# Kernel optimization log

Measured on AMD Instinct MI355X. Metric: run time of the kernel, lower is better.

## Reference

```python
import jax, jax.numpy as jnp
import numpy as np
import math

N_EMBD = 2048
N_HEAD = 16
HEAD_DIM = N_EMBD // N_HEAD  # 128
K = 8
P = 2
B = 1
T = 2048
EPS = 1e-6


def _rms_norm(x):
    return x * jax.lax.rsqrt(jnp.mean(x * x, axis=-1, keepdims=True) + EPS)


def _rope(x, cos, sin):
    # x: [B, T, H, D]; cos/sin: [T, D//2]
    d = x.shape[-1] // 2
    x1, x2 = x[..., :d], x[..., d:]
    c = cos[None, :, None, :]
    s = sin[None, :, None, :]
    return jnp.concatenate([x1 * c + x2 * s, -x1 * s + x2 * c], axis=-1)


def setup_inputs() -> dict:
    key = jax.random.key(0)
    ks = jax.random.split(key, 8)
    x = jax.random.normal(ks[0], (B, T, N_EMBD), jnp.float32)
    half = HEAD_DIM // 2
    inv_freq = 1.0 / (10000.0 ** (np.arange(half, dtype=np.float32) / half))
    ang = np.arange(T, dtype=np.float32)[:, None] * inv_freq[None, :]
    cos = jnp.asarray(np.cos(ang), jnp.float32)
    sin = jnp.asarray(np.sin(ang), jnp.float32)
    sc = 1.0 / math.sqrt(N_EMBD)
    Wq = jax.random.normal(ks[1], (N_EMBD, N_EMBD), jnp.float32) * sc
    Wk = jax.random.normal(ks[2], (N_EMBD, N_EMBD), jnp.float32) * sc
    Wv = jax.random.normal(ks[3], (N_EMBD, N_EMBD), jnp.float32) * sc
    Wproj = jax.random.normal(ks[4], (N_EMBD, N_EMBD), jnp.float32) * sc
    scd = 1.0 / math.sqrt(HEAD_DIM)
    Wdq = jax.random.normal(ks[5], (K, HEAD_DIM), jnp.float32) * scd
    Wdk = jax.random.normal(ks[6], (K, HEAD_DIM), jnp.float32) * scd
    return {"x": x, "cos": cos, "sin": sin, "Wq": Wq, "Wk": Wk, "Wv": Wv, "Wproj": Wproj, "Wdq": Wdq, "Wdk": Wdk}


def reference(x, cos, sin, Wq, Wk, Wv, Wproj, Wdq, Wdk):
    Bq, Tq, C = x.shape
    q = (x @ Wq.T).reshape(Bq, Tq, N_HEAD, HEAD_DIM)
    k = (x @ Wk.T).reshape(Bq, Tq, N_HEAD, HEAD_DIM)
    v = (x @ Wv.T).reshape(Bq, Tq, N_HEAD, HEAD_DIM)
    q = _rms_norm(_rope(q, cos, sin))
    k = _rms_norm(_rope(k, cos, sin))
    q = jnp.swapaxes(q, 1, 2)  # [B,H,T,D]
    k = jnp.swapaxes(k, 1, 2)
    v = jnp.swapaxes(v, 1, 2)
    # base-p digits in {0..p-1}; p=2 -> bits
    qd = jnp.floor(jax.nn.sigmoid(jnp.einsum('bhtd,kd->bhtk', q, Wdq)) * (P - 0.01)).astype(jnp.int32)
    kd = jnp.floor(jax.nn.sigmoid(jnp.einsum('bhtd,kd->bhtk', k, Wdk)) * (P - 0.01)).astype(jnp.int32)
    # lcp >= K-1  <=>  first K-1 digits all equal; pack them into one code
    pw = (P ** jnp.arange(K - 1)).astype(jnp.int32)  # [K-1]
    qc = jnp.sum(qd[..., : K - 1] * pw, axis=-1)  # [B,H,T]
    kc = jnp.sum(kd[..., : K - 1] * pw, axis=-1)
    lcp_mask = qc[..., :, None] == kc[..., None, :]  # [B,H,Tq,Tk]
    causal = jnp.tril(jnp.ones((Tq, Tq), dtype=bool))
    mask = lcp_mask & causal
    scores = jnp.einsum('bhqd,bhkd->bhqk', q, k) * (1.0 / math.sqrt(HEAD_DIM))
    s = jnp.where(mask, scores, -1e30)
    w = jax.nn.softmax(s, axis=-1)
    w = jnp.where(mask, w, 0.0)
    any_valid = jnp.any(mask, axis=-1, keepdims=True)
    w = jnp.where(any_valid, w, 0.0)  # fully-masked rows -> zero output (torch gives NaN)
    y = jnp.einsum('bhqk,bhkd->bhqd', w, v)
    y = jnp.swapaxes(y, 1, 2).reshape(Bq, Tq, C)
    return y @ Wproj.T
```

## Files before the change

### kernel.cpp

```cpp
#include <hip/hip_runtime.h>
#include <hip/hip_bf16.h>
#include <math.h>

#define T 2048
#define C 2048
#define NH 16
#define HD 128
#define SCALE 0.08838834764831845f
#define WL_CAP 2048
#define MARG 1e-4f

typedef short s16x8 __attribute__((ext_vector_type(8)));
typedef float f32x4 __attribute__((ext_vector_type(4)));
typedef _Float16 f16;
typedef f16 f16x8 __attribute__((ext_vector_type(8)));

__device__ __forceinline__ float wave_sum(float v) {
  #pragma unroll
  for (int o = 32; o > 0; o >>= 1) v += __shfl_xor(v, o, 64);
  return v;
}
__device__ __forceinline__ unsigned short f2bf(float f) {
  unsigned u = __float_as_uint(f);
  u += 0x7FFFu + ((u >> 16) & 1u);
  return (unsigned short)(u >> 16);
}

__global__ __launch_bounds__(256) void to_bf16(const float* __restrict__ in,
                                               unsigned short* __restrict__ outp,
                                               int n4) {
  int i = blockIdx.x * blockDim.x + threadIdx.x;
  const int stride = gridDim.x * blockDim.x;
  for (; i < n4; i += stride) {
    float4 v = ((const float4*)in)[i];
    ushort4 o;
    o.x = f2bf(v.x); o.y = f2bf(v.y); o.z = f2bf(v.z); o.w = f2bf(v.w);
    ((ushort4*)outp)[i] = o;
  }
}

#define PRESC 4096.0f
#define S0F 5.9604644775390625e-8f
#define S1F 2.9103830456733704e-11f
#define S2F 1.4210854715202004e-14f

__global__ __launch_bounds__(256) void split_f16(const float* __restrict__ in,
                                                 unsigned short* __restrict__ hip_,
                                                 unsigned short* __restrict__ lop,
                                                 int n4) {
  int i = blockIdx.x * blockDim.x + threadIdx.x;
  const int stride = gridDim.x * blockDim.x;
  for (; i < n4; i += stride) {
    float4 v = ((const float4*)in)[i];
    float s0 = v.x * PRESC, s1 = v.y * PRESC, s2 = v.z * PRESC, s3 = v.w * PRESC;
    union { f16 h[4]; ushort4 u; } H, L;
    H.h[0] = (f16)s0; H.h[1] = (f16)s1; H.h[2] = (f16)s2; H.h[3] = (f16)s3;
    L.h[0] = (f16)((s0 - (float)H.h[0]) * 2048.0f);
    L.h[1] = (f16)((s1 - (float)H.h[1]) * 2048.0f);
    L.h[2] = (f16)((s2 - (float)H.h[2]) * 2048.0f);
    L.h[3] = (f16)((s3 - (float)H.h[3]) * 2048.0f);
    ((ushort4*)hip_)[i] = H.u;
    ((ushort4*)lop)[i] = L.u;
  }
}

__global__ __launch_bounds__(256) void to_f16h(const float* __restrict__ in,
                                               unsigned short* __restrict__ outp,
                                               int n4) {
  int i = blockIdx.x * blockDim.x + threadIdx.x;
  const int stride = gridDim.x * blockDim.x;
  for (; i < n4; i += stride) {
    float4 v = ((const float4*)in)[i];
    union { f16 h[4]; ushort4 u; } H;
    H.h[0] = (f16)(v.x * PRESC); H.h[1] = (f16)(v.y * PRESC);
    H.h[2] = (f16)(v.z * PRESC); H.h[3] = (f16)(v.w * PRESC);
    ((ushort4*)outp)[i] = H.u;
  }
}

#define SBM 64
#define SBN 128
#define SBK 32

__global__ __launch_bounds__(256, 3) void gemm_qk2(const unsigned short* __restrict__ xhp,
                                                   const unsigned short* __restrict__ xlp,
                                                   const unsigned short* __restrict__ wqh,
                                                   const unsigned short* __restrict__ wql,
                                                   const unsigned short* __restrict__ wkh,
                                                   const unsigned short* __restrict__ wkl,
                                                   float* __restrict__ Qo,
                                                   float* __restrict__ Ko) {
  const unsigned short* __restrict__ Ahp = xhp;
  const unsigned short* __restrict__ Alp = xlp;
  const unsigned short* __restrict__ Bhp = blockIdx.z ? wkh : wqh;
  const unsigned short* __restrict__ Blp = blockIdx.z ? wkl : wql;
  float* __restrict__ Cc = blockIdx.z ? Ko : Qo;
  __shared__ unsigned short Ah[2][SBM * SBK];
  __shared__ unsigned short Av[2][SBM * SBK];
  __shared__ unsigned short Bh[2][SBN * SBK];
  __shared__ unsigned short Bv[2][SBN * SBK];
  const int tid = threadIdx.x;
  const int bm = blockIdx.x * SBM;
  const int bn = blockIdx.y * SBN;
  const int wv = tid >> 6, lane = tid & 63;
  const int wm = wv & 1, wn = wv >> 1;
  const int lrow = lane & 15, lquad = lane >> 4;

  const int a_row = tid >> 2, qg = tid & 3;
  const int a_qs = qg ^ ((a_row >> 1) & 3);
  const int b_row0 = tid >> 2;
  const int b_qs = qg ^ ((b_row0 >> 1) & 3);

  f32x4 acc[2][2][4];
  #pragma unroll
  for (int g = 0; g < 2; ++g)
    #pragma unroll
    for (int i = 0; i < 2; ++i)
      #pragma unroll
      for (int j = 0; j < 4; ++j) acc[g][i][j] = (f32x4){0.f, 0.f, 0.f, 0.f};

  {
    uint4 aH = *(const uint4*)(Ahp + (size_t)(bm + a_row) * C + qg * 8);
    uint4 aL = *(const uint4*)(Alp + (size_t)(bm + a_row) * C + qg * 8);
    uint4 b0H = *(const uint4*)(Bhp + (size_t)(bn + b_row0) * C + qg * 8);
    uint4 b0L = *(const uint4*)(Blp + (size_t)(bn + b_row0) * C + qg * 8);
    uint4 b1H = *(const uint4*)(Bhp + (size_t)(bn + 64 + b_row0) * C + qg * 8);
    uint4 b1L = *(const uint4*)(Blp + (size_t)(bn + 64 + b_row0) * C + qg * 8);
    *(uint4*)&Ah[0][a_row * SBK + a_qs * 8] = aH;
    *(uint4*)&Av[0][a_row * SBK + a_qs * 8] = aL;
    *(uint4*)&Bh[0][b_row0 * SBK + b_qs * 8] = b0H;
    *(uint4*)&Bv[0][b_row0 * SBK + b_qs * 8] = b0L;
    *(uint4*)&Bh[0][(64 + b_row0) * SBK + b_qs * 8] = b1H;
    *(uint4*)&Bv[0][(64 + b_row0) * SBK + b_qs * 8] = b1L;
  }
  __syncthreads();

  const int niter = C / SBK;
  for (int it = 0; it < niter; ++it) {
    const int cur = it & 1;
    const bool has = (it + 1) < niter;
    uint4 aHn, aLn, b0Hn, b0Ln, b1Hn, b1Ln;
    if (has) {
      const int k0 = (it + 1) * SBK;
      aHn = *(const uint4*)(Ahp + (size_t)(bm + a_row) * C + k0 + qg * 8);
      aLn = *(const uint4*)(Alp + (size_t)(bm + a_row) * C + k0 + qg * 8);
      b0Hn = *(const uint4*)(Bhp + (size_t)(bn + b_row0) * C + k0 + qg * 8);
      b0Ln = *(const uint4*)(Blp + (size_t)(bn + b_row0) * C + k0 + qg * 8);
      b1Hn = *(const uint4*)(Bhp + (size_t)(bn + 64 + b_row0) * C + k0 + qg * 8);
      b1Ln = *(const uint4*)(Blp + (size_t)(bn + 64 + b_row0) * C + k0 + qg * 8);
    }
    f16x8 ah[2], av[2], bh[4], bv[4];
    #pragma unroll
    for (int mi = 0; mi < 2; ++mi) {
      const int r = wm * 32 + mi * 16 + lrow;
      const int q = lquad ^ ((r >> 1) & 3);
      ah[mi] = *(const f16x8*)&Ah[cur][r * SBK + q * 8];
      av[mi] = *(const f16x8*)&Av[cur][r * SBK + q * 8];
    }
    #pragma unroll
    for (int ni = 0; ni < 4; ++ni) {
      const int r = wn * 64 + ni * 16 + lrow;
      const int q = lquad ^ ((r >> 1) & 3);
      bh[ni] = *(const f16x8*)&Bh[cur][r * SBK + q * 8];
      bv[ni] = *(const f16x8*)&Bv[cur][r * SBK + q * 8];
    }
    #pragma unroll
    for (int mi = 0; mi < 2; ++mi)
      #pragma unroll
      for (int ni = 0; ni < 4; ++ni) {
        acc[0][mi][ni] = __builtin_amdgcn_mfma_f32_16x16x32_f16(ah[mi], bh[ni], acc[0][mi][ni], 0, 0, 0);
        acc[1][mi][ni] = __builtin_amdgcn_mfma_f32_16x16x32_f16(ah[mi], bv[ni], acc[1][mi][ni], 0, 0, 0);
        acc[1][mi][ni] = __builtin_amdgcn_mfma_f32_16x16x32_f16(av[mi], bh[ni], acc[1][mi][ni], 0, 0, 0);
      }
    if (has) {
      const int nxt = cur ^ 1;
      *(uint4*)&Ah[nxt][a_row * SBK + a_qs * 8] = aHn;
      *(uint4*)&Av[nxt][a_row * SBK + a_qs * 8] = aLn;
      *(uint4*)&Bh[nxt][b_row0 * SBK + b_qs * 8] = b0Hn;
      *(uint4*)&Bv[nxt][b_row0 * SBK + b_qs * 8] = b0Ln;
      *(uint4*)&Bh[nxt][(64 + b_row0) * SBK + b_qs * 8] = b1Hn;
      *(uint4*)&Bv[nxt][(64 + b_row0) * SBK + b_qs * 8] = b1Ln;
    }
    __syncthreads();
  }
  #pragma unroll
  for (int mi = 0; mi < 2; ++mi)
    #pragma unroll
    for (int ni = 0; ni < 4; ++ni)
      #pragma unroll
      for (int r = 0; r < 4; ++r) {
        int row = bm + wm * 32 + mi * 16 + lquad * 4 + r;
        int col = bn + wn * 64 + ni * 16 + lrow;
        Cc[(size_t)row * C + col] = acc[0][mi][ni][r] * S0F + acc[1][mi][ni][r] * S1F;
      }
}

__global__ __launch_bounds__(256) void gemm_h1(const unsigned short* __restrict__ A,
                                               const unsigned short* __restrict__ B,
                                               float* __restrict__ Cc) {
  __shared__ unsigned short Ah[2][SBM * SBK];
  __shared__ unsigned short Bh[2][SBN * SBK];
  const int tid = threadIdx.x;
  const int bm = blockIdx.x * SBM;
  const int bn = blockIdx.y * SBN;
  const int wv = tid >> 6, lane = tid & 63;
  const int wm = wv & 1, wn = wv >> 1;
  const int lrow = lane & 15, lquad = lane >> 4;

  const int a_row = tid >> 2, qg = tid & 3;
  const int a_qs = qg ^ ((a_row >> 1) & 3);
  const int b_row0 = tid >> 2;
  const int b_qs = qg ^ ((b_row0 >> 1) & 3);

  f32x4 acc[2][4];
  #pragma unroll
  for (int i = 0; i < 2; ++i)
    #pragma unroll
    for (int j = 0; j < 4; ++j) acc[i][j] = (f32x4){0.f, 0.f, 0.f, 0.f};

  {
    uint4 av = *(const uint4*)(A + (size_t)(bm + a_row) * C + qg * 8);
    uint4 b0 = *(const uint4*)(B + (size_t)(bn + b_row0) * C + qg * 8);
    uint4 b1 = *(const uint4*)(B + (size_t)(bn + 64 + b_row0) * C + qg * 8);
    *(uint4*)&Ah[0][a_row * SBK + a_qs * 8] = av;
    *(uint4*)&Bh[0][b_row0 * SBK + b_qs * 8] = b0;
    *(uint4*)&Bh[0][(64 + b_row0) * SBK + b_qs * 8] = b1;
  }
  __syncthreads();

  const int niter = C / SBK;
  for (int it = 0; it < niter; ++it) {
    const int cur = it & 1;
    const bool has = (it + 1) < niter;
    uint4 avn, b0n, b1n;
    if (has) {
      const int k0 = (it + 1) * SBK;
      avn = *(const uint4*)(A + (size_t)(bm + a_row) * C + k0 + qg * 8);
      b0n = *(const uint4*)(B + (size_t)(bn + b_row0) * C + k0 + qg * 8);
      b1n = *(const uint4*)(B + (size_t)(bn + 64 + b_row0) * C + k0 + qg * 8);
    }
    f16x8 af[2], bfr[4];
    #pragma unroll
    for (int mi = 0; mi < 2; ++mi) {
      const int r = wm * 32 + mi * 16 + lrow;
      const int q = lquad ^ ((r >> 1) & 3);
      af[mi] = *(const f16x8*)&Ah[cur][r * SBK + q * 8];
    }
    #pragma unroll
    for (int ni = 0; ni < 4; ++ni) {
      const int r = wn * 64 + ni * 16 + lrow;
      const int q = lquad ^ ((r >> 1) & 3);
      bfr[ni] = *(const f16x8*)&Bh[cur][r * SBK + q * 8];
    }
    #pragma unroll
    for (int mi = 0; mi < 2; ++mi)
      #pragma unroll
      for (int ni = 0; ni < 4; ++ni)
        acc[mi][ni] = __builtin_amdgcn_mfma_f32_16x16x32_f16(af[mi], bfr[ni], acc[mi][ni], 0, 0, 0);
    if (has) {
      const int nxt = cur ^ 1;
      *(uint4*)&Ah[nxt][a_row * SBK + a_qs * 8] = avn;
      *(uint4*)&Bh[nxt][b_row0 * SBK + b_qs * 8] = b0n;
      *(uint4*)&Bh[nxt][(64 + b_row0) * SBK + b_qs * 8] = b1n;
    }
    __syncthreads();
  }
  #pragma unroll
  for (int mi = 0; mi < 2; ++mi)
    #pragma unroll
    for (int ni = 0; ni < 4; ++ni)
      #pragma unroll
      for (int r = 0; r < 4; ++r) {
        int row = bm + wm * 32 + mi * 16 + lquad * 4 + r;
        int col = bn + wn * 64 + ni * 16 + lrow;
        Cc[(size_t)row * C + col] = acc[mi][ni][r] * S0F;
      }
}

__device__ __forceinline__ void split8(const float4 v0, const float4 v1,
                                       uint4& hi, uint4& lo) {
  float s[8] = {v0.x * PRESC, v0.y * PRESC, v0.z * PRESC, v0.w * PRESC,
                v1.x * PRESC, v1.y * PRESC, v1.z * PRESC, v1.w * PRESC};
  union { uint4 u; f16 h[8]; } H, L;
  #pragma unroll
  for (int i = 0; i < 8; ++i) {
    f16 h2 = (f16)s[i];
    float d = s[i] - (float)h2;
    H.h[i] = h2;
    L.h[i] = (f16)(d * 2048.0f);
  }
  hi = H.u; lo = L.u;
}

__global__ __launch_bounds__(256, 2) void gemm_qk_split16(const float* __restrict__ A,
                                                          const float* __restrict__ Wq,
                                                          const float* __restrict__ Wk,
                                                          float* __restrict__ Qo,
                                                          float* __restrict__ Ko) {
  const float* __restrict__ Bw = blockIdx.z ? Wk : Wq;
  float* __restrict__ Cc = blockIdx.z ? Ko : Qo;
  __shared__ unsigned short Ah[2][SBM * SBK];
  __shared__ unsigned short Av[2][SBM * SBK];
  __shared__ unsigned short Bh[2][SBN * SBK];
  __shared__ unsigned short Bv[2][SBN * SBK];
  const int tid = threadIdx.x;
  const int bm = blockIdx.x * SBM;
  const int bn = blockIdx.y * SBN;
  const int wv = tid >> 6, lane = tid & 63;
  const int wm = wv & 1, wn = wv >> 1;
  const int lrow = lane & 15, lquad = lane >> 4;

  const int a_row = tid >> 2, qg = tid & 3;
  const int a_qs = qg ^ ((a_row >> 1) & 3);
  const int b_row0 = tid >> 2;
  const int b_qs = qg ^ ((b_row0 >> 1) & 3);

  f32x4 acc[3][2][4];
  #pragma unroll
  for (int g = 0; g < 3; ++g)
    #pragma unroll
    for (int i = 0; i < 2; ++i)
      #pragma unroll
      for (int j = 0; j < 4; ++j) acc[g][i][j] = (f32x4){0.f, 0.f, 0.f, 0.f};

  {
    const float* pA  = A  + (size_t)(bm + a_row) * C + qg * 8;
    const float* pB0 = Bw + (size_t)(bn + b_row0) * C + qg * 8;
    const float* pB1 = Bw + (size_t)(bn + 64 + b_row0) * C + qg * 8;
    uint4 h, l;
    split8(*(const float4*)pA, *(const float4*)(pA + 4), h, l);
    *(uint4*)&Ah[0][a_row * SBK + a_qs * 8] = h;
    *(uint4*)&Av[0][a_row * SBK + a_qs * 8] = l;
    split8(*(const float4*)pB0, *(const float4*)(pB0 + 4), h, l);
    *(uint4*)&Bh[0][b_row0 * SBK + b_qs * 8] = h;
    *(uint4*)&Bv[0][b_row0 * SBK + b_qs * 8] = l;
    split8(*(const float4*)pB1, *(const float4*)(pB1 + 4), h, l);
    *(uint4*)&Bh[0][(64 + b_row0) * SBK + b_qs * 8] = h;
    *(uint4*)&Bv[0][(64 + b_row0) * SBK + b_qs * 8] = l;
  }
  __syncthreads();

  const int niter = C / SBK;
  for (int it = 0; it < niter; ++it) {
    const int cur = it & 1;
    const bool has = (it + 1) < niter;
    float4 a0n, a1n, b00n, b01n, b10n, b11n;
    if (has) {
      const int k0 = (it + 1) * SBK;
      const float* pA  = A  + (size_t)(bm + a_row) * C + k0 + qg * 8;
      const float* pB0 = Bw + (size_t)(bn + b_row0) * C + k0 + qg * 8;
      const float* pB1 = Bw + (size_t)(bn + 64 + b_row0) * C + k0 + qg * 8;
      a0n = *(const float4*)pA;   a1n = *(const float4*)(pA + 4);
      b00n = *(const float4*)pB0; b01n = *(const float4*)(pB0 + 4);
      b10n = *(const float4*)pB1; b11n = *(const float4*)(pB1 + 4);
    }
    f16x8 ah[2], av[2], bh[4], bv[4];
    #pragma unroll
    for (int mi = 0; mi < 2; ++mi) {
      const int r = wm * 32 + mi * 16 + lrow;
      const int q = lquad ^ ((r >> 1) & 3);
      ah[mi] = *(const f16x8*)&Ah[cur][r * SBK + q * 8];
      av[mi] = *(const f16x8*)&Av[cur][r * SBK + q * 8];
    }
    #pragma unroll
    for (int ni = 0; ni < 4; ++ni) {
      const int r = wn * 64 + ni * 16 + lrow;
      const int q = lquad ^ ((r >> 1) & 3);
      bh[ni] = *(const f16x8*)&Bh[cur][r * SBK + q * 8];
      bv[ni] = *(const f16x8*)&Bv[cur][r * SBK + q * 8];
    }
    #pragma unroll
    for (int mi = 0; mi < 2; ++mi)
      #pragma unroll
      for (int ni = 0; ni < 4; ++ni) {
        acc[0][mi][ni] = __builtin_amdgcn_mfma_f32_16x16x32_f16(ah[mi], bh[ni], acc[0][mi][ni], 0, 0, 0);
        acc[1][mi][ni] = __builtin_amdgcn_mfma_f32_16x16x32_f16(ah[mi], bv[ni], acc[1][mi][ni], 0, 0, 0);
        acc[1][mi][ni] = __builtin_amdgcn_mfma_f32_16x16x32_f16(av[mi], bh[ni], acc[1][mi][ni], 0, 0, 0);
        acc[2][mi][ni] = __builtin_amdgcn_mfma_f32_16x16x32_f16(av[mi], bv[ni], acc[2][mi][ni], 0, 0, 0);
      }
    if (has) {
      const int nxt = cur ^ 1;
      uint4 h, l;
      split8(a0n, a1n, h, l);
      *(uint4*)&Ah[nxt][a_row * SBK + a_qs * 8] = h;
      *(uint4*)&Av[nxt][a_row * SBK + a_qs * 8] = l;
      split8(b00n, b01n, h, l);
      *(uint4*)&Bh[nxt][b_row0 * SBK + b_qs * 8] = h;
      *(uint4*)&Bv[nxt][b_row0 * SBK + b_qs * 8] = l;
      split8(b10n, b11n, h, l);
      *(uint4*)&Bh[nxt][(64 + b_row0) * SBK + b_qs * 8] = h;
      *(uint4*)&Bv[nxt][(64 + b_row0) * SBK + b_qs * 8] = l;
    }
    __syncthreads();
  }
  #pragma unroll
  for (int mi = 0; mi < 2; ++mi)
    #pragma unroll
    for (int ni = 0; ni < 4; ++ni)
      #pragma unroll
      for (int r = 0; r < 4; ++r) {
        int row = bm + wm * 32 + mi * 16 + lquad * 4 + r;
        int col = bn + wn * 64 + ni * 16 + lrow;
        float v = acc[0][mi][ni][r] * S0F + (acc[1][mi][ni][r] * S1F + acc[2][mi][ni][r] * S2F);
        Cc[(size_t)row * C + col] = v;
      }
}

#define VBM 64
#define VBN 128
#define VBK 32

__global__ __launch_bounds__(256) void gemm_bf16n(const unsigned short* __restrict__ A,
                                                  const unsigned short* __restrict__ B,
                                                  float* __restrict__ Cc) {
  __shared__ unsigned short Al[2][VBM * VBK];
  __shared__ unsigned short Bl[2][VBN * VBK];
  const int tid = threadIdx.x;
  const int bm = blockIdx.x * VBM;
  const int bn = blockIdx.y * VBN;
  const int wv = tid >> 6, lane = tid & 63;
  const int wm = wv & 1, wn = wv >> 1;
  const int lrow = lane & 15, lquad = lane >> 4;

  const int a_row = tid >> 2, qg = tid & 3;
  const int a_qs = qg ^ ((a_row >> 1) & 3);
  const int b_row0 = tid >> 2;
  const int b_qs = qg ^ ((b_row0 >> 1) & 3);

  f32x4 acc[2][4];
  #pragma unroll
  for (int i = 0; i < 2; ++i)
    #pragma unroll
    for (int j = 0; j < 4; ++j) acc[i][j] = (f32x4){0.f, 0.f, 0.f, 0.f};

  {
    uint4 av = *(const uint4*)(A + (size_t)(bm + a_row) * C + qg * 8);
    uint4 b0 = *(const uint4*)(B + (size_t)(bn + b_row0) * C + qg * 8);
    uint4 b1 = *(const uint4*)(B + (size_t)(bn + 64 + b_row0) * C + qg * 8);
    *(uint4*)&Al[0][a_row * VBK + a_qs * 8] = av;
    *(uint4*)&Bl[0][b_row0 * VBK + b_qs * 8] = b0;
    *(uint4*)&Bl[0][(64 + b_row0) * VBK + b_qs * 8] = b1;
  }
  __syncthreads();

  const int niter = C / VBK;
  for (int it = 0; it < niter; ++it) {
    const int cur = it & 1;
    const bool has = (it + 1) < niter;
    uint4 avn, b0n, b1n;
    if (has) {
      const int k0 = (it + 1) * VBK;
      avn = *(const uint4*)(A + (size_t)(bm + a_row) * C + k0 + qg * 8);
      b0n = *(const uint4*)(B + (size_t)(bn + b_row0) * C + k0 + qg * 8);
      b1n = *(const uint4*)(B + (size_t)(bn + 64 + b_row0) * C + k0 + qg * 8);
    }
    s16x8 af[2], bfr[4];
    #pragma unroll
    for (int mi = 0; mi < 2; ++mi) {
      const int r = wm * 32 + mi * 16 + lrow;
      const int q = lquad ^ ((r >> 1) & 3);
      af[mi] = *(const s16x8*)&Al[cur][r * VBK + q * 8];
    }
    #pragma unroll
    for (int ni = 0; ni < 4; ++ni) {
      const int r = wn * 64 + ni * 16 + lrow;
      const int q = lquad ^ ((r >> 1) & 3);
      bfr[ni] = *(const s16x8*)&Bl[cur][r * VBK + q * 8];
    }
    #pragma unroll
    for (int mi = 0; mi < 2; ++mi)
      #pragma unroll
      for (int ni = 0; ni < 4; ++ni)
        acc[mi][ni] = __builtin_amdgcn_mfma_f32_16x16x32_bf16(af[mi], bfr[ni], acc[mi][ni], 0, 0, 0);
    if (has) {
      const int nxt = cur ^ 1;
      *(uint4*)&Al[nxt][a_row * VBK + a_qs * 8] = avn;
      *(uint4*)&Bl[nxt][b_row0 * VBK + b_qs * 8] = b0n;
      *(uint4*)&Bl[nxt][(64 + b_row0) * VBK + b_qs * 8] = b1n;
    }
    __syncthreads();
  }
  #pragma unroll
  for (int mi = 0; mi < 2; ++mi)
    #pragma unroll
    for (int ni = 0; ni < 4; ++ni)
      #pragma unroll
      for (int r = 0; r < 4; ++r) {
        int row = bm + wm * 32 + mi * 16 + lquad * 4 + r;
        int col = bn + wn * 64 + ni * 16 + lrow;
        Cc[(size_t)row * C + col] = acc[mi][ni][r];
      }
}

__global__ void zero_ctr(int* __restrict__ ctr) {
  if (threadIdx.x == 0) ctr[0] = 0;
}

__global__ __launch_bounds__(256) void rope_fused(float* __restrict__ Qb,
                                                  float* __restrict__ Kb,
                                                  const float* __restrict__ cosb,
                                                  const float* __restrict__ sinb,
                                                  const float* __restrict__ Wdq,
                                                  const float* __restrict__ Wdk,
                                                  int* __restrict__ qcodes,
                                                  int* __restrict__ kcodes,
                                                  int* __restrict__ wl,
                                                  int* __restrict__ ctr) {
  float* __restrict__ buf = blockIdx.y ? Kb : Qb;
  const float* __restrict__ Wd = blockIdx.y ? Wdk : Wdq;
  int* __restrict__ codes = blockIdx.y ? kcodes : qcodes;
  int wave = (blockIdx.x << 2) + (threadIdx.x >> 6);
  int lane = threadIdx.x & 63;
  int t = wave / NH, h = wave % NH;
  size_t base = (size_t)t * C + h * HD;
  float x1 = buf[base + lane];
  float x2 = buf[base + lane + 64];
  float c = cosb[t * 64 + lane];
  float s = sinb[t * 64 + lane];
  float r1 = x1 * c + x2 * s;
  float r2 = x2 * c - x1 * s;
  float ss = wave_sum(r1 * r1 + r2 * r2);
  float inv = 1.0f / sqrtf(ss * (1.0f / 128.0f) + 1e-6f);
  r1 *= inv; r2 *= inv;
  buf[base + lane] = r1;
  buf[base + lane + 64] = r2;
  int code = 0;
  bool marg = false;
  #pragma unroll
  for (int kk = 0; kk < 7; ++kk) {
    float z = r1 * Wd[kk * HD + lane] + r2 * Wd[kk * HD + lane + 64];
    z = wave_sum(z);
    float sig = 1.0f / (1.0f + expf(-z));
    float d = sig * 1.99f - 1.0f;
    if (d >= 0.f) code |= (1 << kk);
    marg |= (fabsf(d) < MARG);
  }
  if (lane == 0) {
    codes[h * T + t] = code;
    if (marg) {
      int i = atomicAdd(ctr, 1);
      if (i < WL_CAP) wl[i] = ((int)blockIdx.y << 15) | (h << 11) | t;
    }
  }
}

__global__ __launch_bounds__(64) void fix_codes(const float* __restrict__ x,
                                                const float* __restrict__ Wq,
                                                const float* __restrict__ Wk,
                                                const float* __restrict__ cosb,
                                                const float* __restrict__ sinb,
                                                const float* __restrict__ Wdq,
                                                const float* __restrict__ Wdk,
                                                int* __restrict__ qc,
                                                int* __restrict__ kc,
                                                const int* __restrict__ wl,
                                                const int* __restrict__ ctr) {
  const int n = min(ctr[0], WL_CAP);
  const int lane = threadIdx.x;
  for (int e = blockIdx.x; e < n; e += gridDim.x) {
    const int ent = wl[e];
    const int isK = ent >> 15;
    const int h = (ent >> 11) & 15;
    const int t = ent & 2047;
    const float* __restrict__ W  = isK ? Wk : Wq;
    const float* __restrict__ Wd = isK ? Wdk : Wdq;
    int* __restrict__ codes = isK ? kc : qc;

    const float* xr = x + (size_t)t * C;
    const float* w0 = W + (size_t)(h * HD + lane) * C;
    const float* w1 = W + (size_t)(h * HD + lane + 64) * C;
    float p0[4] = {0.f, 0.f, 0.f, 0.f};
    float p1[4] = {0.f, 0.f, 0.f, 0.f};
    for (int k = 0; k < C; k += 4) {
      float4 xv = *(const float4*)(xr + k);
      float4 a = *(const float4*)(w0 + k);
      float4 b = *(const float4*)(w1 + k);
      p0[0] += xv.x * a.x; p0[1] += xv.y * a.y;
      p0[2] += xv.z * a.z; p0[3] += xv.w * a.w;
      p1[0] += xv.x * b.x; p1[1] += xv.y * b.y;
      p1[2] += xv.z * b.z; p1[3] += xv.w * b.w;
    }
    float x1 = (p0[0] + p0[1]) + (p0[2] + p0[3]);
    float x2 = (p1[0] + p1[1]) + (p1[2] + p1[3]);
    float c = cosb[t * 64 + lane];
    float s = sinb[t * 64 + lane];
    float r1 = x1 * c + x2 * s;
    float r2 = x2 * c - x1 * s;
    float ss = wave_sum(r1 * r1 + r2 * r2);
    float inv = 1.0f / sqrtf(ss * (1.0f / 128.0f) + 1e-6f);
    r1 *= inv; r2 *= inv;
    int code = 0;
    #pragma unroll
    for (int kk = 0; kk < 7; ++kk) {
      float z = r1 * Wd[kk * HD + lane] + r2 * Wd[kk * HD + lane + 64];
      z = wave_sum(z);
      float sig = 1.0f / (1.0f + expf(-z));
      if (sig * 1.99f >= 1.0f) code |= (1 << kk);
    }
    if (lane == 0) codes[h * T + t] = code;
  }
}

__global__ __launch_bounds__(256) void attn_sparse(const float* __restrict__ Q,
                                                   const float* __restrict__ Kn,
                                                   const float* __restrict__ V,
                                                   const int* __restrict__ qc,
                                                   const int* __restrict__ kc,
                                                   float* __restrict__ Y) {
  const int tid = threadIdx.x;
  const int lane = tid & 63;
  const int wave_id = blockIdx.x * 4 + (tid >> 6);
  const int h = wave_id & (NH - 1);
  const int qrow = wave_id >> 4;
  const size_t hb = (size_t)h * HD;

  const float q0 = Q[(size_t)qrow * C + hb + lane];
  const float q1 = Q[(size_t)qrow * C + hb + lane + 64];
  const int qcode = qc[h * T + qrow];
  const int* kch = kc + h * T;

  float m = -1e30f, l = 0.f, acc0 = 0.f, acc1 = 0.f;

  const int nchunks = (qrow >> 6) + 1;
  int kcj = kch[lane];
  for (int ci = 0; ci < nchunks; ++ci) {
    const int j0 = ci << 6;
    const int cur = kcj;
    if (ci + 1 < nchunks) kcj = kch[j0 + 64 + lane];
    unsigned long long mask = __ballot((cur == qcode) && (j0 + lane <= qrow));
    while (mask) {
      const int j = j0 + (__ffsll((long long)mask) - 1);
      mask &= mask - 1;
      const float* kr = Kn + (size_t)j * C + hb;
      const float* vr = V + (size_t)j * C + hb;
      const float k0v = kr[lane], k1v = kr[lane + 64];
      const float v0 = vr[lane], v1 = vr[lane + 64];
      const float s = wave_sum(q0 * k0v + q1 * k1v) * SCALE;
      const float m_new = fmaxf(m, s);
      const float alpha = __expf(m - m_new);
      const float p = __expf(s - m_new);
      l = l * alpha + p;
      acc0 = acc0 * alpha + p * v0;
      acc1 = acc1 * alpha + p * v1;
      m = m_new;
    }
  }
  const float invl = (l > 0.f) ? 1.0f / l : 0.f;
  Y[(size_t)qrow * C + hb + lane] = acc0 * invl;
  Y[(size_t)qrow * C + hb + lane + 64] = acc1 * invl;
}

extern "C" void kernel_launch(void* const* d_in, const int* in_sizes, int n_in,
                              void* d_out, int out_size, void* d_ws, size_t ws_size,
                              hipStream_t stream) {
  (void)in_sizes; (void)n_in; (void)out_size;
  const float* x     = (const float*)d_in[0];
  const float* cosb  = (const float*)d_in[1];
  const float* sinb  = (const float*)d_in[2];
  const float* Wq    = (const float*)d_in[3];
  const float* Wk    = (const float*)d_in[4];
  const float* Wv    = (const float*)d_in[5];
  const float* Wproj = (const float*)d_in[6];
  const float* Wdq   = (const float*)d_in[7];
  const float* Wdk   = (const float*)d_in[8];
  float* out = (float*)d_out;

  const size_t MB = 1024 * 1024;
  char* ws = (char*)d_ws;
  const int n4 = T * C / 4;

  if (ws_size >= (size_t)64 * MB) {
    unsigned short* xh  = (unsigned short*)(ws);
    unsigned short* xl  = (unsigned short*)(ws + 8 * MB);
    unsigned short* wqh = (unsigned short*)(ws + 16 * MB);
    unsigned short* wql = (unsigned short*)(ws + 24 * MB);
    unsigned short* wkh = (unsigned short*)(ws + 32 * MB);
    unsigned short* wkl = (unsigned short*)(ws + 40 * MB);
    float* K = (float*)(ws + 48 * MB);
    unsigned short* wvh = (unsigned short*)(ws + 16 * MB);
    float* V = (float*)(ws + 24 * MB);
    int* qc  = (int*)(ws + 40 * MB);
    int* kc  = qc + NH * T;
    int* ctr = kc + NH * T;
    int* wl  = ctr + 16;
    float* Y = (float*)(ws);
    unsigned short* yh  = (unsigned short*)(ws + 16 * MB);
    unsigned short* wph = (unsigned short*)(ws + 24 * MB);
    float* Q = out;

    split_f16<<<2048, 256, 0, stream>>>(x, xh, xl, n4);
    split_f16<<<2048, 256, 0, stream>>>(Wq, wqh, wql, n4);
    split_f16<<<2048, 256, 0, stream>>>(Wk, wkh, wkl, n4);
    gemm_qk2<<<dim3(T / SBM, C / SBN, 2), 256, 0, stream>>>(xh, xl, wqh, wql, wkh, wkl, Q, K);
    to_f16h<<<2048, 256, 0, stream>>>(Wv, wvh, n4);
    gemm_h1<<<dim3(T / SBM, C / SBN), 256, 0, stream>>>(xh, wvh, V);
    zero_ctr<<<1, 64, 0, stream>>>(ctr);
    rope_fused<<<dim3(T * NH / 4, 2), 256, 0, stream>>>(Q, K, cosb, sinb, Wdq, Wdk, qc, kc, wl, ctr);
    fix_codes<<<256, 64, 0, stream>>>(x, Wq, Wk, cosb, sinb, Wdq, Wdk, qc, kc, wl, ctr);
    attn_sparse<<<T * NH / 4, 256, 0, stream>>>(Q, K, V, qc, kc, Y);
    to_f16h<<<2048, 256, 0, stream>>>(Y, yh, n4);
    to_f16h<<<2048, 256, 0, stream>>>(Wproj, wph, n4);
    gemm_h1<<<dim3(T / SBM, C / SBN), 256, 0, stream>>>(yh, wph, out);
  } else {
    float* Kbuf = (float*)ws;
    float* V    = (float*)(ws + 16 * MB);
    float* Y    = (float*)(ws + 32 * MB);
    unsigned short* Wbf = (unsigned short*)(ws + 48 * MB);
    unsigned short* xbf = (unsigned short*)Y;
    unsigned short* Ybf = (unsigned short*)Kbuf;
    float* Q    = out;
    int* qc  = (int*)(Wbf + (size_t)T * C);
    int* kc  = qc + NH * T;
    int* ctr = kc + NH * T;
    int* wl  = ctr + 16;

    to_bf16<<<2048, 256, 0, stream>>>(x, xbf, n4);
    to_bf16<<<2048, 256, 0, stream>>>(Wv, Wbf, n4);
    gemm_bf16n<<<dim3(T / VBM, C / VBN), 256, 0, stream>>>(xbf, Wbf, V);
    gemm_qk_split16<<<dim3(T / SBM, C / SBN, 2), 256, 0, stream>>>(x, Wq, Wk, Q, Kbuf);
    zero_ctr<<<1, 64, 0, stream>>>(ctr);
    rope_fused<<<dim3(T * NH / 4, 2), 256, 0, stream>>>(Q, Kbuf, cosb, sinb, Wdq, Wdk, qc, kc, wl, ctr);
    fix_codes<<<256, 64, 0, stream>>>(x, Wq, Wk, cosb, sinb, Wdq, Wdk, qc, kc, wl, ctr);
    attn_sparse<<<T * NH / 4, 256, 0, stream>>>(Q, Kbuf, V, qc, kc, Y);
    to_bf16<<<2048, 256, 0, stream>>>(Y, Ybf, n4);
    to_bf16<<<2048, 256, 0, stream>>>(Wproj, Wbf, n4);
    gemm_bf16n<<<dim3(T / VBM, C / VBN), 256, 0, stream>>>(Ybf, Wbf, out);
  }
}
```

Baseline: 502.3 us.

## Fuse Q/K split-precision GEMM into one tile sharing x loads, merge conversion launches

Replaces the two-pass Q/K GEMM, which used a z-grid dimension, with one kernel. Each block covers 128 rows of x and 64 columns of both Wq and Wk, so the x hi/lo tile is loaded once and reused for both outputs. The three split_f16 launches become one 2D launch, and the two to_f16h conversions before the output projection become one, cutting kernel launch overhead. The cost is more accumulator registers, with launch bounds lowered to 2 blocks per SM, which may reduce occupancy. Small bounds-hardening tweaks are also made to the worklist indexing.

```diff
diff --git a/kernel.cpp b/kernel.cpp
--- a/kernel.cpp
+++ b/kernel.cpp
@@ -44,6 +44,17 @@
 #define S1F 2.9103830456733704e-11f
 #define S2F 1.4210854715202004e-14f
 
+__device__ __forceinline__ void split4(float4 v, ushort4& hi, ushort4& lo) {
+  float s0 = v.x * PRESC, s1 = v.y * PRESC, s2 = v.z * PRESC, s3 = v.w * PRESC;
+  union { f16 h[4]; ushort4 u; } H, L;
+  H.h[0] = (f16)s0; H.h[1] = (f16)s1; H.h[2] = (f16)s2; H.h[3] = (f16)s3;
+  L.h[0] = (f16)((s0 - (float)H.h[0]) * 2048.0f);
+  L.h[1] = (f16)((s1 - (float)H.h[1]) * 2048.0f);
+  L.h[2] = (f16)((s2 - (float)H.h[2]) * 2048.0f);
+  L.h[3] = (f16)((s3 - (float)H.h[3]) * 2048.0f);
+  hi = H.u; lo = L.u;
+}
+
 __global__ __launch_bounds__(256) void split_f16(const float* __restrict__ in,
                                                  unsigned short* __restrict__ hip_,
                                                  unsigned short* __restrict__ lop,
@@ -51,16 +62,35 @@
   int i = blockIdx.x * blockDim.x + threadIdx.x;
   const int stride = gridDim.x * blockDim.x;
   for (; i < n4; i += stride) {
-    float4 v = ((const float4*)in)[i];
-    float s0 = v.x * PRESC, s1 = v.y * PRESC, s2 = v.z * PRESC, s3 = v.w * PRESC;
-    union { f16 h[4]; ushort4 u; } H, L;
-    H.h[0] = (f16)s0; H.h[1] = (f16)s1; H.h[2] = (f16)s2; H.h[3] = (f16)s3;
-    L.h[0] = (f16)((s0 - (float)H.h[0]) * 2048.0f);
-    L.h[1] = (f16)((s1 - (float)H.h[1]) * 2048.0f);
-    L.h[2] = (f16)((s2 - (float)H.h[2]) * 2048.0f);
-    L.h[3] = (f16)((s3 - (float)H.h[3]) * 2048.0f);
-    ((ushort4*)hip_)[i] = H.u;
-    ((ushort4*)lop)[i] = L.u;
+    ushort4 h, l;
+    split4(((const float4*)in)[i], h, l);
+    ((ushort4*)hip_)[i] = h;
+    ((ushort4*)lop)[i] = l;
+  }
+}
+
+__global__ __launch_bounds__(256) void pre_split3(const float* __restrict__ x,
+                                                  const float* __restrict__ Wq,
+                                                  const float* __restrict__ Wk,
+                                                  unsigned short* __restrict__ xh,
+                                                  unsigned short* __restrict__ xl,
+                                                  unsigned short* __restrict__ wqh,
+                                                  unsigned short* __restrict__ wql,
+                                                  unsigned short* __restrict__ wkh,
+                                                  unsigned short* __restrict__ wkl,
+                                                  int n4) {
+  const float* __restrict__ in;
+  unsigned short *oh, *ol;
+  if (blockIdx.y == 0)      { in = x;  oh = xh;  ol = xl;  }
+  else if (blockIdx.y == 1) { in = Wq; oh = wqh; ol = wql; }
+  else                      { in = Wk; oh = wkh; ol = wkl; }
+  int i = blockIdx.x * blockDim.x + threadIdx.x;
+  const int stride = gridDim.x * blockDim.x;
+  for (; i < n4; i += stride) {
+    ushort4 h, l;
+    split4(((const float4*)in)[i], h, l);
+    ((ushort4*)oh)[i] = h;
+    ((ushort4*)ol)[i] = l;
   }
 }
 
@@ -78,11 +108,29 @@
   }
 }
 
+__global__ __launch_bounds__(256) void post_h2(const float* __restrict__ Y,
+                                               const float* __restrict__ Wproj,
+                                               unsigned short* __restrict__ yh,
+                                               unsigned short* __restrict__ wph,
+                                               int n4) {
+  const float* __restrict__ in = blockIdx.y ? Wproj : Y;
+  unsigned short* __restrict__ outp = blockIdx.y ? wph : yh;
+  int i = blockIdx.x * blockDim.x + threadIdx.x;
+  const int stride = gridDim.x * blockDim.x;
+  for (; i < n4; i += stride) {
+    float4 v = ((const float4*)in)[i];
+    union { f16 h[4]; ushort4 u; } H;
+    H.h[0] = (f16)(v.x * PRESC); H.h[1] = (f16)(v.y * PRESC);
+    H.h[2] = (f16)(v.z * PRESC); H.h[3] = (f16)(v.w * PRESC);
+    ((ushort4*)outp)[i] = H.u;
+  }
+}
+
 #define SBM 64
 #define SBN 128
 #define SBK 32
 
-__global__ __launch_bounds__(256, 3) void gemm_qk2(const unsigned short* __restrict__ xhp,
+__global__ __launch_bounds__(256, 2) void gemm_qkf(const unsigned short* __restrict__ xhp,
                                                    const unsigned short* __restrict__ xlp,
                                                    const unsigned short* __restrict__ wqh,
                                                    const unsigned short* __restrict__ wql,
@@ -90,108 +138,111 @@
                                                    const unsigned short* __restrict__ wkl,
                                                    float* __restrict__ Qo,
                                                    float* __restrict__ Ko) {
-  const unsigned short* __restrict__ Ahp = xhp;
-  const unsigned short* __restrict__ Alp = xlp;
-  const unsigned short* __restrict__ Bhp = blockIdx.z ? wkh : wqh;
-  const unsigned short* __restrict__ Blp = blockIdx.z ? wkl : wql;
-  float* __restrict__ Cc = blockIdx.z ? Ko : Qo;
-  __shared__ unsigned short Ah[2][SBM * SBK];
-  __shared__ unsigned short Av[2][SBM * SBK];
-  __shared__ unsigned short Bh[2][SBN * SBK];
-  __shared__ unsigned short Bv[2][SBN * SBK];
+  __shared__ unsigned short Ah[2][128 * 32];
+  __shared__ unsigned short Av[2][128 * 32];
+  __shared__ unsigned short Bh[2][128 * 32];
+  __shared__ unsigned short Bv[2][128 * 32];
   const int tid = threadIdx.x;
-  const int bm = blockIdx.x * SBM;
-  const int bn = blockIdx.y * SBN;
+  const int bm = blockIdx.x * 128;
+  const int bn = blockIdx.y * 64;
   const int wv = tid >> 6, lane = tid & 63;
   const int wm = wv & 1, wn = wv >> 1;
   const int lrow = lane & 15, lquad = lane >> 4;
 
-  const int a_row = tid >> 2, qg = tid & 3;
-  const int a_qs = qg ^ ((a_row >> 1) & 3);
-  const int b_row0 = tid >> 2;
-  const int b_qs = qg ^ ((b_row0 >> 1) & 3);
-
-  f32x4 acc[2][2][4];
-  #pragma unroll
-  for (int g = 0; g < 2; ++g)
-    #pragma unroll
-    for (int i = 0; i < 2; ++i)
-      #pragma unroll
-      for (int j = 0; j < 4; ++j) acc[g][i][j] = (f32x4){0.f, 0.f, 0.f, 0.f};
+  const int sr = tid >> 2, qg = tid & 3;
+  const int qs = qg ^ ((sr >> 1) & 3);
+
+  f32x4 acc0[4][4], acc1[4][4];
+  #pragma unroll
+  for (int i = 0; i < 4; ++i)
+    #pragma unroll
+    for (int j = 0; j < 4; ++j) {
+      acc0[i][j] = (f32x4){0.f, 0.f, 0.f, 0.f};
+      acc1[i][j] = (f32x4){0.f, 0.f, 0.f, 0.f};
+    }
 
   {
-    uint4 aH = *(const uint4*)(Ahp + (size_t)(bm + a_row) * C + qg * 8);
-    uint4 aL = *(const uint4*)(Alp + (size_t)(bm + a_row) * C + qg * 8);
-    uint4 b0H = *(const uint4*)(Bhp + (size_t)(bn + b_row0) * C + qg * 8);
-    uint4 b0L = *(const uint4*)(Blp + (size_t)(bn + b_row0) * C + qg * 8);
-    uint4 b1H = *(const uint4*)(Bhp + (size_t)(bn + 64 + b_row0) * C + qg * 8);
-    uint4 b1L = *(const uint4*)(Blp + (size_t)(bn + 64 + b_row0) * C + qg * 8);
-    *(uint4*)&Ah[0][a_row * SBK + a_qs * 8] = aH;
-    *(uint4*)&Av[0][a_row * SBK + a_qs * 8] = aL;
-    *(uint4*)&Bh[0][b_row0 * SBK + b_qs * 8] = b0H;
-    *(uint4*)&Bv[0][b_row0 * SBK + b_qs * 8] = b0L;
-    *(uint4*)&Bh[0][(64 + b_row0) * SBK + b_qs * 8] = b1H;
-    *(uint4*)&Bv[0][(64 + b_row0) * SBK + b_qs * 8] = b1L;
+    uint4 a0H = *(const uint4*)(xhp + (size_t)(bm + sr) * C + qg * 8);
+    uint4 a0L = *(const uint4*)(xlp + (size_t)(bm + sr) * C + qg * 8);
+    uint4 a1H = *(const uint4*)(xhp + (size_t)(bm + 64 + sr) * C + qg * 8);
+    uint4 a1L = *(const uint4*)(xlp + (size_t)(bm + 64 + sr) * C + qg * 8);
+    uint4 bqH = *(const uint4*)(wqh + (size_t)(bn + sr) * C + qg * 8);
+    uint4 bqL = *(const uint4*)(wql + (size_t)(bn + sr) * C + qg * 8);
+    uint4 bkH = *(const uint4*)(wkh + (size_t)(bn + sr) * C + qg * 8);
+    uint4 bkL = *(const uint4*)(wkl + (size_t)(bn + sr) * C + qg * 8);
+    *(uint4*)&Ah[0][sr * 32 + qs * 8] = a0H;
+    *(uint4*)&Av[0][sr * 32 + qs * 8] = a0L;
+    *(uint4*)&Ah[0][(64 + sr) * 32 + qs * 8] = a1H;
+    *(uint4*)&Av[0][(64 + sr) * 32 + qs * 8] = a1L;
+    *(uint4*)&Bh[0][sr * 32 + qs * 8] = bqH;
+    *(uint4*)&Bv[0][sr * 32 + qs * 8] = bqL;
+    *(uint4*)&Bh[0][(64 + sr) * 32 + qs * 8] = bkH;
+    *(uint4*)&Bv[0][(64 + sr) * 32 + qs * 8] = bkL;
   }
   __syncthreads();
 
-  const int niter = C / SBK;
+  const int niter = C / 32;
   for (int it = 0; it < niter; ++it) {
     const int cur = it & 1;
     const bool has = (it + 1) < niter;
-    uint4 aHn, aLn, b0Hn, b0Ln, b1Hn, b1Ln;
+    uint4 a0H, a0L, a1H, a1L, bqH, bqL, bkH, bkL;
     if (has) {
-      const int k0 = (it + 1) * SBK;
-      aHn = *(const uint4*)(Ahp + (size_t)(bm + a_row) * C + k0 + qg * 8);
-      aLn = *(const uint4*)(Alp + (size_t)(bm + a_row) * C + k0 + qg * 8);
-      b0Hn = *(const uint4*)(Bhp + (size_t)(bn + b_row0) * C + k0 + qg * 8);
-      b0Ln = *(const uint4*)(Blp + (size_t)(bn + b_row0) * C + k0 + qg * 8);
-      b1Hn = *(const uint4*)(Bhp + (size_t)(bn + 64 + b_row0) * C + k0 + qg * 8);
-      b1Ln = *(const uint4*)(Blp + (size_t)(bn + 64 + b_row0) * C + k0 + qg * 8);
-    }
-    f16x8 ah[2], av[2], bh[4], bv[4];
-    #pragma unroll
-    for (int mi = 0; mi < 2; ++mi) {
-      const int r = wm * 32 + mi * 16 + lrow;
+      const int k0 = (it + 1) * 32;
+      a0H = *(const uint4*)(xhp + (size_t)(bm + sr) * C + k0 + qg * 8);
+      a0L = *(const uint4*)(xlp + (size_t)(bm + sr) * C + k0 + qg * 8);
+      a1H = *(const uint4*)(xhp + (size_t)(bm + 64 + sr) * C + k0 + qg * 8);
+      a1L = *(const uint4*)(xlp + (size_t)(bm + 64 + sr) * C + k0 + qg * 8);
+      bqH = *(const uint4*)(wqh + (size_t)(bn + sr) * C + k0 + qg * 8);
+      bqL = *(const uint4*)(wql + (size_t)(bn + sr) * C + k0 + qg * 8);
+      bkH = *(const uint4*)(wkh + (size_t)(bn + sr) * C + k0 + qg * 8);
+      bkL = *(const uint4*)(wkl + (size_t)(bn + sr) * C + k0 + qg * 8);
+    }
+    f16x8 ah[4], av[4], bh[4], bv[4];
+    #pragma unroll
+    for (int mi = 0; mi < 4; ++mi) {
+      const int r = wm * 64 + mi * 16 + lrow;
       const int q = lquad ^ ((r >> 1) & 3);
-      ah[mi] = *(const f16x8*)&Ah[cur][r * SBK + q * 8];
-      av[mi] = *(const f16x8*)&Av[cur][r * SBK + q * 8];
+      ah[mi] = *(const f16x8*)&Ah[cur][r * 32 + q * 8];
+      av[mi] = *(const f16x8*)&Av[cur][r * 32 + q * 8];
     }
     #pragma unroll
     for (int ni = 0; ni < 4; ++ni) {
       const int r = wn * 64 + ni * 16 + lrow;
       const int q = lquad ^ ((r >> 1) & 3);
-      bh[ni] = *(const f16x8*)&Bh[cur][r * SBK + q * 8];
-      bv[ni] = *(const f16x8*)&Bv[cur][r * SBK + q * 8];
-    }
-    #pragma unroll
-    for (int mi = 0; mi < 2; ++mi)
+      bh[ni] = *(const f16x8*)&Bh[cur][r * 32 + q * 8];
+      bv[ni] = *(const f16x8*)&Bv[cur][r * 32 + q * 8];
+    }
+    #pragma unroll
+    for (int mi = 0; mi < 4; ++mi)
       #pragma unroll
       for (int ni = 0; ni < 4; ++ni) {
-        acc[0][mi][ni] = __builtin_amdgcn_mfma_f32_16x16x32_f16(ah[mi], bh[ni], acc[0][mi][ni], 0, 0, 0);
-        acc[1][mi][ni] = __builtin_amdgcn_mfma_f32_16x16x32_f16(ah[mi], bv[ni], acc[1][mi][ni], 0, 0, 0);
-        acc[1][mi][ni] = __builtin_amdgcn_mfma_f32_16x16x32_f16(av[mi], bh[ni], acc[1][mi][ni], 0, 0, 0);
+        acc0[mi][ni] = __builtin_amdgcn_mfma_f32_16x16x32_f16(ah[mi], bh[ni], acc0[mi][ni], 0, 0, 0);
+        acc1[mi][ni] = __builtin_amdgcn_mfma_f32_16x16x32_f16(ah[mi], bv[ni], acc1[mi][ni], 0, 0, 0);
+        acc1[mi][ni] = __builtin_amdgcn_mfma_f32_16x16x32_f16(av[mi], bh[ni], acc1[mi][ni], 0, 0, 0);
       }
     if (has) {
       const int nxt = cur ^ 1;
-      *(uint4*)&Ah[nxt][a_row * SBK + a_qs * 8] = aHn;
-      *(uint4*)&Av[nxt][a_row * SBK + a_qs * 8] = aLn;
-      *(uint4*)&Bh[nxt][b_row0 * SBK + b_qs * 8] = b0Hn;
-      *(uint4*)&Bv[nxt][b_row0 * SBK + b_qs * 8] = b0Ln;
-      *(uint4*)&Bh[nxt][(64 + b_row0) * SBK + b_qs * 8] = b1Hn;
-      *(uint4*)&Bv[nxt][(64 + b_row0) * SBK + b_qs * 8] = b1Ln;
+      *(uint4*)&Ah[nxt][sr * 32 + qs * 8] = a0H;
+      *(uint4*)&Av[nxt][sr * 32 + qs * 8] = a0L;
+      *(uint4*)&Ah[nxt][(64 + sr) * 32 + qs * 8] = a1H;
+      *(uint4*)&Av[nxt][(64 + sr) * 32 + qs * 8] = a1L;
+      *(uint4*)&Bh[nxt][sr * 32 + qs * 8] = bqH;
+      *(uint4*)&Bv[nxt][sr * 32 + qs * 8] = bqL;
+      *(uint4*)&Bh[nxt][(64 + sr) * 32 + qs * 8] = bkH;
+      *(uint4*)&Bv[nxt][(64 + sr) * 32 + qs * 8] = bkL;
     }
     __syncthreads();
   }
-  #pragma unroll
-  for (int mi = 0; mi < 2; ++mi)
+  float* __restrict__ Cc = wn ? Ko : Qo;
+  #pragma unroll
+  for (int mi = 0; mi < 4; ++mi)
     #pragma unroll
     for (int ni = 0; ni < 4; ++ni)
       #pragma unroll
       for (int r = 0; r < 4; ++r) {
-        int row = bm + wm * 32 + mi * 16 + lquad * 4 + r;
-        int col = bn + wn * 64 + ni * 16 + lrow;
-        Cc[(size_t)row * C + col] = acc[0][mi][ni][r] * S0F + acc[1][mi][ni][r] * S1F;
+        int row = bm + wm * 64 + mi * 16 + lquad * 4 + r;
+        int col = bn + ni * 16 + lrow;
+        Cc[(size_t)row * C + col] = acc0[mi][ni][r] * S0F + acc1[mi][ni][r] * S1F;
       }
 }
 
@@ -539,7 +590,7 @@
     codes[h * T + t] = code;
     if (marg) {
       int i = atomicAdd(ctr, 1);
-      if (i < WL_CAP) wl[i] = ((int)blockIdx.y << 15) | (h << 11) | t;
+      if ((unsigned)i < (unsigned)WL_CAP) wl[i] = ((int)blockIdx.y << 15) | (h << 11) | t;
     }
   }
 }
@@ -555,11 +606,11 @@
                                                 int* __restrict__ kc,
                                                 const int* __restrict__ wl,
                                                 const int* __restrict__ ctr) {
-  const int n = min(ctr[0], WL_CAP);
+  const int n = min(max(ctr[0], 0), WL_CAP);
   const int lane = threadIdx.x;
   for (int e = blockIdx.x; e < n; e += gridDim.x) {
     const int ent = wl[e];
-    const int isK = ent >> 15;
+    const int isK = (ent >> 15) & 1;
     const int h = (ent >> 11) & 15;
     const int t = ent & 2047;
     const float* __restrict__ W  = isK ? Wk : Wq;
@@ -688,18 +739,15 @@
     unsigned short* wph = (unsigned short*)(ws + 24 * MB);
     float* Q = out;
 
-    split_f16<<<2048, 256, 0, stream>>>(x, xh, xl, n4);
-    split_f16<<<2048, 256, 0, stream>>>(Wq, wqh, wql, n4);
-    split_f16<<<2048, 256, 0, stream>>>(Wk, wkh, wkl, n4);
-    gemm_qk2<<<dim3(T / SBM, C / SBN, 2), 256, 0, stream>>>(xh, xl, wqh, wql, wkh, wkl, Q, K);
+    pre_split3<<<dim3(1024, 3), 256, 0, stream>>>(x, Wq, Wk, xh, xl, wqh, wql, wkh, wkl, n4);
+    zero_ctr<<<1, 64, 0, stream>>>(ctr);
+    gemm_qkf<<<dim3(T / 128, C / 64), 256, 0, stream>>>(xh, xl, wqh, wql, wkh, wkl, Q, K);
     to_f16h<<<2048, 256, 0, stream>>>(Wv, wvh, n4);
     gemm_h1<<<dim3(T / SBM, C / SBN), 256, 0, stream>>>(xh, wvh, V);
-    zero_ctr<<<1, 64, 0, stream>>>(ctr);
     rope_fused<<<dim3(T * NH / 4, 2), 256, 0, stream>>>(Q, K, cosb, sinb, Wdq, Wdk, qc, kc, wl, ctr);
     fix_codes<<<256, 64, 0, stream>>>(x, Wq, Wk, cosb, sinb, Wdq, Wdk, qc, kc, wl, ctr);
     attn_sparse<<<T * NH / 4, 256, 0, stream>>>(Q, K, V, qc, kc, Y);
-    to_f16h<<<2048, 256, 0, stream>>>(Y, yh, n4);
-    to_f16h<<<2048, 256, 0, stream>>>(Wproj, wph, n4);
+    post_h2<<<dim3(1024, 2), 256, 0, stream>>>(Y, Wproj, yh, wph, n4);
     gemm_h1<<<dim3(T / SBM, C / SBN), 256, 0, stream>>>(yh, wph, out);
   } else {
     float* Kbuf = (float*)ws;
```

Result: faster. 461.3 us (-8.2%).
